# Kernel tuning notes

Hardware: AMD Instinct MI355X
Metric: run time of the kernel (lower is better)

The kernel has to match this reference:

```python
import jax, jax.numpy as jnp
import numpy as np

NUM_SPECIES = 4
NUM_PAIRS = NUM_SPECIES * (NUM_SPECIES + 1) // 2  # 10 species pairs
RCR = 5.2   # radial cutoff (Angstrom)
RCA = 3.5   # angular cutoff (must be < RCR)
ETA_R = 16.0
SHF_R = jnp.asarray(0.9 + 0.26875 * np.arange(16), dtype=jnp.float32)
ETA_A = 8.0
ZETA = 32.0
SHF_A = jnp.asarray(0.9 + 0.65 * np.arange(4), dtype=jnp.float32)       # 4 angular radial shifts
SHF_Z = jnp.asarray((np.pi / 16.0) * (1.0 + 2.0 * np.arange(8)), dtype=jnp.float32)  # 8 angle sections


def _triu_index(num_species):
    # mirrors AEVComputer._calculate_triu_index
    s1, s2 = np.triu_indices(num_species, 0)
    ret = np.zeros((num_species, num_species), dtype=np.int32)
    ret[s1, s2] = np.arange(len(s1))
    ret[s2, s1] = np.arange(len(s1))
    return jnp.asarray(ret)

TRIU = _triu_index(NUM_SPECIES)


def _fc(d, rc):
    # cosine cutoff; the (d <= rc) validity is applied via masks outside
    return 0.5 * jnp.cos(jnp.pi * d / rc) + 0.5


def _aev(species, coords):
    N, A = species.shape
    dt = coords.dtype
    diff = coords[:, None, :, :] - coords[:, :, None, :]          # (N,i,j,3): r_j - r_i
    eye = jnp.eye(A, dtype=bool)
    d2 = jnp.sum(diff * diff, axis=-1)
    dist = jnp.sqrt(jnp.where(eye, 1.0, d2))                      # (N,i,j), self-distance guarded

    # ---- radial AEV: 0.25 * exp(-EtaR*(d-ShfR)^2) * fc(d), scattered by neighbor species ----
    rmask = (~eye) & (dist <= RCR)
    rad = 0.25 * jnp.exp(-ETA_R * (dist[..., None] - SHF_R) ** 2) * _fc(dist, RCR)[..., None]
    rad = rad * rmask[..., None].astype(dt)                       # (N,i,j,16)
    sp1h = jax.nn.one_hot(species, NUM_SPECIES, dtype=dt)         # (N,j,S)
    radial_aev = jnp.einsum('nijr,njs->nisr', rad, sp1h).reshape(N, A, -1)  # (N,A,64)

    # ---- angular AEV over triples (i; j,k), j,k neighbors of i within RCA ----
    amask = (~eye) & (dist <= RCA)                                # (N,i,j)
    tri = amask[:, :, :, None] & amask[:, :, None, :] & (~eye)[None, None]  # (N,i,j,k), j!=k
    dot = jnp.einsum('nijc,nikc->nijk', diff, diff)
    cos = 0.95 * dot / (dist[:, :, :, None] * dist[:, :, None, :])  # 0.95 stabilizer as in torchani
    theta = jnp.arccos(jnp.clip(cos, -0.95, 0.95))                # (N,i,j,k)
    fcj = _fc(dist, RCA)
    base = 2.0 * fcj[:, :, :, None] * fcj[:, :, None, :] * tri.astype(dt)
    davg = 0.5 * (dist[:, :, :, None] + dist[:, :, None, :])
    f2 = jnp.exp(-ETA_A * (davg[..., None] - SHF_A) ** 2)         # (N,i,j,k,ShfA=4)
    f1 = ((1.0 + jnp.cos(theta[..., None] - SHF_Z)) * 0.5) ** ZETA  # (N,i,j,k,ShfZ=8)
    term = (base[..., None, None] * f2[..., :, None] * f1[..., None, :]).reshape(N, A, A, A, -1)
    pair_idx = TRIU[species[:, :, None], species[:, None, :]]     # (N,j,k)
    pair1h = jax.nn.one_hot(pair_idx, NUM_PAIRS, dtype=dt)        # (N,j,k,P=10)
    # each unordered pair {j,k} is counted once in torchani -> 0.5 * symmetric ordered sum
    angular_aev = 0.5 * jnp.einsum('nijkq,njkp->nipq', term, pair1h).reshape(N, A, -1)  # (N,A,320)

    return jnp.concatenate([radial_aev, angular_aev], axis=-1)    # (N,A,384)


def setup_inputs():
    key = jax.random.key(0)
    k1, k2 = jax.random.split(key)
    N, A, BOX = 16, 64, 12.0
    coords = jax.random.uniform(k1, (N, A, 3), dtype=jnp.float32) * BOX  # atoms in a 12 A box
    species = jax.random.randint(k2, (N, A), 0, NUM_SPECIES)
    return {"species": species, "coords": coords}


def reference(species, coords):
    # SpeciesAEV: (species, aev) with aev shape (N, A, aev_length=384)
    return species, _aev(species, coords)
```

## Files before the change

### kernel.cpp

```cpp
#include <hip/hip_runtime.h>

#define RCR 5.2f
#define RCA 3.5f
#define PI_F 3.14159265358979323846f

__constant__ int c_triu[16] = {0,1,2,3, 1,4,5,6, 2,5,7,8, 3,6,8,9};

__global__ __launch_bounds__(64) void aev_kernel(
    const int* __restrict__ species,
    const float* __restrict__ coords,
    float* __restrict__ out,
    int NA)
{
    const int blk = blockIdx.x;
    const int n   = blk >> 6;
    const int i   = blk & 63;
    const int tid = threadIdx.x;

    __shared__ float sx[64], sy[64], sz[64];
    __shared__ int   ssp[64];
    __shared__ float dxs[64], dys[64], dzs[64], ds[64];
    __shared__ float pre_r[64];
    __shared__ float fca[64];
    __shared__ int   nbr[64];

    const float* c = coords + (size_t)(n * 64) * 3;
    sx[tid]  = c[tid * 3 + 0];
    sy[tid]  = c[tid * 3 + 1];
    sz[tid]  = c[tid * 3 + 2];
    ssp[tid] = species[n * 64 + tid];
    __syncthreads();

    const float xi = sx[i], yi = sy[i], zi = sz[i];
    const float ddx = sx[tid] - xi;
    const float ddy = sy[tid] - yi;
    const float ddz = sz[tid] - zi;
    const float d   = sqrtf(ddx * ddx + ddy * ddy + ddz * ddz);
    dxs[tid] = ddx; dys[tid] = ddy; dzs[tid] = ddz; ds[tid] = d;

    const bool isj = (tid != i);
    pre_r[tid] = (isj && d <= RCR)
                   ? 0.25f * (0.5f * __cosf((PI_F / RCR) * d) + 0.5f) : 0.0f;
    fca[tid]   = 0.5f * __cosf((PI_F / RCA) * d) + 0.5f;

    const bool apred = isj && (d <= RCA);
    const unsigned long long bal = __ballot(apred);
    if (apred) {
        const int pos = __popcll(bal & ((1ull << tid) - 1ull));
        nbr[pos] = tid;
    }
    const int M = __popcll(bal);
    __syncthreads();

    const int   my_s   = tid >> 4;
    const float my_shf = 0.9f + 0.26875f * (float)(tid & 15);
    float racc = 0.0f;
    #pragma unroll 4
    for (int j = 0; j < 64; j++) {
        const float t = ds[j] - my_shf;
        const float e = pre_r[j] * __expf(-16.0f * t * t);
        racc += (ssp[j] == my_s) ? e : 0.0f;
    }

    float acc[5];
    int   my_p[5];
    float my_shfa[5], my_cphi[5], my_sphi[5];
    #pragma unroll
    for (int u = 0; u < 5; u++) {
        const int b = tid + 64 * u;
        my_p[u] = b >> 5;
        const int a = (b >> 3) & 3;
        const int z = b & 7;
        my_shfa[u] = 0.9f + 0.65f * (float)a;
        const float phi = (PI_F / 16.0f) * (float)(1 + 2 * z);
        float sp_, cp_;
        __sincosf(phi, &sp_, &cp_);
        my_cphi[u] = cp_;
        my_sphi[u] = sp_;
        acc[u] = 0.0f;
    }

    for (int jj = 1; jj < M; jj++) {
        const int j = nbr[jj];
        const float dij = ds[j];
        const float xj = dxs[j], yj = dys[j], zj = dzs[j];
        const float fcj = fca[j];
        const int sj4 = ssp[j] * 4;
        for (int kk = 0; kk < jj; kk++) {
            const int k = nbr[kk];
            const float dik = ds[k];
            const float dot = xj * dxs[k] + yj * dys[k] + zj * dzs[k];
            float cosv = 0.95f * dot * __frcp_rn(dij * dik);
            cosv = fminf(0.95f, fmaxf(-0.95f, cosv));
            const float sinv = sqrtf(1.0f - cosv * cosv);
            const float base2 = 2.0f * fcj * fca[k];
            const float davg  = 0.5f * (dij + dik);
            const int   pidx  = c_triu[sj4 + ssp[k]];
            #pragma unroll
            for (int u = 0; u < 5; u++) {
                const float t  = davg - my_shfa[u];
                const float e  = base2 * __expf(-8.0f * t * t);
                const float w  = cosv * my_cphi[u] + sinv * my_sphi[u];
                const float tz = 0.5f + 0.5f * w;
                const float t2 = tz * tz, t4 = t2 * t2, t8 = t4 * t4;
                const float t16 = t8 * t8, t32 = t16 * t16;
                acc[u] += (pidx == my_p[u]) ? e * t32 : 0.0f;
            }
        }
    }

    const int atom = n * 64 + i;
    if (tid == 0) out[atom] = (float)ssp[i];
    float* dstg = out + NA + (size_t)atom * 384;
    dstg[tid] = racc;
    #pragma unroll
    for (int u = 0; u < 5; u++) dstg[64 + tid + 64 * u] = acc[u];
}

extern "C" void kernel_launch(void* const* d_in, const int* in_sizes, int n_in,
                              void* d_out, int out_size, void* d_ws, size_t ws_size,
                              hipStream_t stream) {
    const int*   species = (const int*)d_in[0];
    const float* coords  = (const float*)d_in[1];
    float*       out     = (float*)d_out;
    const int NA = in_sizes[0];
    aev_kernel<<<NA, 64, 0, stream>>>(species, coords, out, NA);
}
```

Before: 76.05 us.

## Parallelize angular triples across threads with shared-memory atomic accumulation

The angular term is restructured so that each thread handles distinct neighbor pairs (j,k), decoded from a flat triangular index, instead of every thread looping over all pairs and evaluating only its own 5 output features. Each pair computes 4 radial and 8 angular factors once and scatters 32 products into a shared-memory accumulator with atomicAdd. This removes the redundant per-thread recomputation of cos, sin and exp for every pair, and the per-feature masking. In exchange it adds 32 shared atomics per pair with possible contention on the same species-pair bins. It also makes the summation order nondeterministic.

```diff
diff --git a/kernel.cpp b/kernel.cpp
--- a/kernel.cpp
+++ b/kernel.cpp
@@ -3,8 +3,6 @@
 #define RCR 5.2f
 #define RCA 3.5f
 #define PI_F 3.14159265358979323846f
-
-__constant__ int c_triu[16] = {0,1,2,3, 1,4,5,6, 2,5,7,8, 3,6,8,9};
 
 __global__ __launch_bounds__(64) void aev_kernel(
     const int* __restrict__ species,
@@ -23,6 +21,7 @@
     __shared__ float pre_r[64];
     __shared__ float fca[64];
     __shared__ int   nbr[64];
+    __shared__ float s_ang[320];
 
     const float* c = coords + (size_t)(n * 64) * 3;
     sx[tid]  = c[tid * 3 + 0];
@@ -50,71 +49,73 @@
         nbr[pos] = tid;
     }
     const int M = __popcll(bal);
+
+    for (int f = tid; f < 320; f += 64) s_ang[f] = 0.0f;
     __syncthreads();
 
     const int   my_s   = tid >> 4;
     const float my_shf = 0.9f + 0.26875f * (float)(tid & 15);
     float racc = 0.0f;
-    #pragma unroll 4
+    #pragma unroll 8
     for (int j = 0; j < 64; j++) {
         const float t = ds[j] - my_shf;
-        const float e = pre_r[j] * __expf(-16.0f * t * t);
-        racc += (ssp[j] == my_s) ? e : 0.0f;
+        racc += (ssp[j] == my_s) ? pre_r[j] * __expf(-16.0f * t * t) : 0.0f;
     }
 
-    float acc[5];
-    int   my_p[5];
-    float my_shfa[5], my_cphi[5], my_sphi[5];
-    #pragma unroll
-    for (int u = 0; u < 5; u++) {
-        const int b = tid + 64 * u;
-        my_p[u] = b >> 5;
-        const int a = (b >> 3) & 3;
-        const int z = b & 7;
-        my_shfa[u] = 0.9f + 0.65f * (float)a;
-        const float phi = (PI_F / 16.0f) * (float)(1 + 2 * z);
-        float sp_, cp_;
-        __sincosf(phi, &sp_, &cp_);
-        my_cphi[u] = cp_;
-        my_sphi[u] = sp_;
-        acc[u] = 0.0f;
+    const float CPHI[8] = { 0.98078528f,  0.83146961f,  0.55557023f,  0.19509032f,
+                           -0.19509032f, -0.55557023f, -0.83146961f, -0.98078528f};
+    const float SPHI[8] = { 0.19509032f,  0.55557023f,  0.83146961f,  0.98078528f,
+                            0.98078528f,  0.83146961f,  0.55557023f,  0.19509032f};
+    const float SHFA[4] = {0.9f, 1.55f, 2.2f, 2.85f};
+
+    const int P = (M * (M - 1)) >> 1;
+    for (int q = tid; q < P; q += 64) {
+        int jj = (int)((1.0f + sqrtf(1.0f + 8.0f * (float)q)) * 0.5f);
+        while (((jj * (jj - 1)) >> 1) > q) --jj;
+        while ((((jj + 1) * jj) >> 1) <= q) ++jj;
+        const int kk = q - ((jj * (jj - 1)) >> 1);
+
+        const int j = nbr[jj], k = nbr[kk];
+        const float dij = ds[j], dik = ds[k];
+        const float dot = dxs[j] * dxs[k] + dys[j] * dys[k] + dzs[j] * dzs[k];
+        float cosv = 0.95f * dot * __builtin_amdgcn_rcpf(dij * dik);
+        cosv = fminf(0.95f, fmaxf(-0.95f, cosv));
+        const float sinv = sqrtf(fmaxf(0.0f, 1.0f - cosv * cosv));
+        const float base2 = 2.0f * fca[j] * fca[k];
+        const float davg  = 0.5f * (dij + dik);
+        const int s1 = ssp[j], s2 = ssp[k];
+        const int smin = (s1 < s2) ? s1 : s2;
+        const int smax = (s1 < s2) ? s2 : s1;
+        const int pidx = ((smin * (7 - smin)) >> 1) + smax;
+
+        float f2[4];
+        #pragma unroll
+        for (int a = 0; a < 4; a++) {
+            const float t = davg - SHFA[a];
+            f2[a] = base2 * __expf(-8.0f * t * t);
+        }
+        float t32z[8];
+        #pragma unroll
+        for (int z = 0; z < 8; z++) {
+            const float w  = 0.5f + 0.5f * (cosv * CPHI[z] + sinv * SPHI[z]);
+            const float t2 = w * w, t4 = t2 * t2, t8 = t4 * t4, t16 = t8 * t8;
+            t32z[z] = t16 * t16;
+        }
+        float* dst = &s_ang[pidx * 32];
+        #pragma unroll
+        for (int a = 0; a < 4; a++)
+            #pragma unroll
+            for (int z = 0; z < 8; z++)
+                atomicAdd(&dst[a * 8 + z], f2[a] * t32z[z]);
     }
-
-    for (int jj = 1; jj < M; jj++) {
-        const int j = nbr[jj];
-        const float dij = ds[j];
-        const float xj = dxs[j], yj = dys[j], zj = dzs[j];
-        const float fcj = fca[j];
-        const int sj4 = ssp[j] * 4;
-        for (int kk = 0; kk < jj; kk++) {
-            const int k = nbr[kk];
-            const float dik = ds[k];
-            const float dot = xj * dxs[k] + yj * dys[k] + zj * dzs[k];
-            float cosv = 0.95f * dot * __frcp_rn(dij * dik);
-            cosv = fminf(0.95f, fmaxf(-0.95f, cosv));
-            const float sinv = sqrtf(1.0f - cosv * cosv);
-            const float base2 = 2.0f * fcj * fca[k];
-            const float davg  = 0.5f * (dij + dik);
-            const int   pidx  = c_triu[sj4 + ssp[k]];
-            #pragma unroll
-            for (int u = 0; u < 5; u++) {
-                const float t  = davg - my_shfa[u];
-                const float e  = base2 * __expf(-8.0f * t * t);
-                const float w  = cosv * my_cphi[u] + sinv * my_sphi[u];
-                const float tz = 0.5f + 0.5f * w;
-                const float t2 = tz * tz, t4 = t2 * t2, t8 = t4 * t4;
-                const float t16 = t8 * t8, t32 = t16 * t16;
-                acc[u] += (pidx == my_p[u]) ? e * t32 : 0.0f;
-            }
-        }
-    }
+    __syncthreads();
 
     const int atom = n * 64 + i;
     if (tid == 0) out[atom] = (float)ssp[i];
     float* dstg = out + NA + (size_t)atom * 384;
     dstg[tid] = racc;
     #pragma unroll
-    for (int u = 0; u < 5; u++) dstg[64 + tid + 64 * u] = acc[u];
+    for (int u = 0; u < 5; u++) dstg[64 + tid + 64 * u] = s_ang[tid + 64 * u];
 }
 
 extern "C" void kernel_launch(void* const* d_in, const int* in_sizes, int n_in,
```

New measurement: 67.81 us. 10.8% less time.
